# Optimization experiments

Measured on AMD Instinct MI355X. Metric: run time of the kernel, lower is better.

The kernel has to match this reference:

```python
import jax, jax.numpy as jnp
import numpy as np

B, S, D = 4, 2048, 1024
N_EXPERTS, EXPERT_SIZE = 16, 256
WIDTH = N_EXPERTS * EXPERT_SIZE  # 4096


def setup_inputs() -> dict:
    key = jax.random.key(0)
    k_x, k_w1, k_w2, k_g = jax.random.split(key, 4)
    x = jax.random.normal(k_x, (B, S, D), dtype=jnp.float32)
    # Linear params, fan-in scaled init
    w1 = jax.random.normal(k_w1, (D, WIDTH), dtype=jnp.float32) / np.sqrt(D).astype(np.float32)
    b1 = jnp.zeros((WIDTH,), dtype=jnp.float32)
    w2 = jax.random.normal(k_w2, (WIDTH, D), dtype=jnp.float32) / np.sqrt(WIDTH).astype(np.float32)
    b2 = jnp.zeros((D,), dtype=jnp.float32)
    return {"x": x, "w1": w1, "b1": b1, "w2": w2, "b2": b2}


def reference(x, w1, b1, w2, b2):
    # NOTE: the original module computes expert-choice routing tensors
    # (gate einsum -> topk -> one_hot -> identity matmul 'gather'), but the
    # returned value is ONLY the dense FFN applied to x; all routing results
    # are dead code with no effect on the output. Faithful output math:
    h = jax.nn.relu(jnp.einsum('bsd,dw->bsw', x, w1) + b1)  # [B,S,WIDTH]
    return jnp.einsum('bsw,wd->bsd', h, w2) + b2            # [B,S,D]
```

## Files before the change

### kernel.cpp

```cpp
#include <hip/hip_runtime.h>
#include <hip/hip_bf16.h>


typedef __bf16 bf16;
typedef __bf16 bf16x4 __attribute__((ext_vector_type(4)));
typedef __bf16 bf16x8 __attribute__((ext_vector_type(8)));
typedef float  f32x4  __attribute__((ext_vector_type(4)));

#define BM 256
#define BN 128
#define BK 64

__device__ __forceinline__ void gload_lds16(const bf16* g, bf16* l) {
    __builtin_amdgcn_global_load_lds(
        (const __attribute__((address_space(1))) unsigned int*)g,
        (__attribute__((address_space(3))) unsigned int*)l,
        16, 0, 0);
}

__device__ __forceinline__ void transpose_tile(
    const float* __restrict__ in, bf16* __restrict__ out,
    int K, int N, int bx, int by, int t, bf16 (*tile)[72])
{
    const int k0 = by * 64;
    const int n0 = bx * 64;
    const int lr = t >> 4;
    const int lc = (t & 15) << 2;
#pragma unroll
    for (int p = 0; p < 4; ++p) {
        int k = p * 16 + lr;
        float4 v = *(const float4*)(in + (size_t)(k0 + k) * N + n0 + lc);
        tile[lc + 0][k] = (bf16)v.x;
        tile[lc + 1][k] = (bf16)v.y;
        tile[lc + 2][k] = (bf16)v.z;
        tile[lc + 3][k] = (bf16)v.w;
    }
    __syncthreads();
    const int wr = t >> 3;
    const int wc = (t & 7) << 3;
#pragma unroll
    for (int p = 0; p < 2; ++p) {
        int n = p * 32 + wr;
        *(bf16x8*)(out + (size_t)(n0 + n) * K + k0 + wc) =
            *(const bf16x8*)&tile[n][wc];
    }
}

__global__ __launch_bounds__(256) void prep(
    const float* __restrict__ x,  bf16* __restrict__ xb,
    const float* __restrict__ w1, bf16* __restrict__ w1t,
    const float* __restrict__ w2, bf16* __restrict__ w2t)
{
    __shared__ __align__(16) bf16 tile[64][72];
    const int b = blockIdx.x;
    const int t = threadIdx.x;
    if (b < 8192) {
        int i = b * 256 + t;
        float4 v = ((const float4*)x)[i];
        bf16x4 o;
        o.x = (bf16)v.x; o.y = (bf16)v.y; o.z = (bf16)v.z; o.w = (bf16)v.w;
        ((bf16x4*)xb)[i] = o;
    } else if (b < 9216) {
        int b2 = b - 8192;
        transpose_tile(w1, w1t, 1024, 4096, b2 & 63, b2 >> 6, t, tile);
    } else {
        int b2 = b - 9216;
        transpose_tile(w2, w2t, 4096, 1024, b2 & 15, b2 >> 4, t, tile);
    }
}

template <int FUSE_RELU_BF16>
__global__ __launch_bounds__(256, 2) void gemm_bt(
    const bf16* __restrict__ A, const bf16* __restrict__ Bt,
    const float* __restrict__ bias, void* __restrict__ Cout,
    int M, int N, int K, int nx)
{
    __shared__ __align__(16) bf16 As[BM * BK];
    __shared__ __align__(16) bf16 Bs[BN * BK];

    const int lid = blockIdx.x;
    const int xcd = lid & 7;
    const int j   = lid >> 3;
    const int bx  = j % nx;
    const int by  = (j / nx) * 8 + xcd;

    const int tid  = threadIdx.x;
    const int wave = tid >> 6;
    const int lane = tid & 63;

    const int l8  = lane >> 3;
    const int c8  = lane & 7;
    const int swc = (c8 ^ l8) << 3;
    const size_t K_ = (size_t)K;

    const bf16* gA[8]; const bf16* gB[4];
#pragma unroll
    for (int g = 0; g < 8; ++g)
        gA[g] = A + ((size_t)by * BM + wave * 64 + g * 8 + l8) * K_ + swc;
#pragma unroll
    for (int g = 0; g < 4; ++g)
        gB[g] = Bt + ((size_t)bx * BN + wave * 32 + g * 8 + l8) * K_ + swc;
    bf16* lA0 = &As[(wave * 64) * BK] + lane * 8;
    bf16* lB0 = &Bs[(wave * 32) * BK] + lane * 8;

    const int wm   = (wave >> 1) << 7;
    const int wn   = (wave & 1) << 6;
    const int quad = lane >> 4;
    const int r    = lane & 15;
    const int r7   = lane & 7;

    f32x4 acc[8][4] = {};

    for (int k0 = 0; k0 < K; k0 += BK) {
        __syncthreads();
#pragma unroll
        for (int g = 0; g < 8; ++g) {
            gload_lds16(gA[g], lA0 + g * (8 * BK));
            gA[g] += BK;
        }
#pragma unroll
        for (int g = 0; g < 4; ++g) {
            gload_lds16(gB[g], lB0 + g * (8 * BK));
            gB[g] += BK;
        }
        __syncthreads();

#pragma unroll
        for (int h = 0; h < 2; ++h) {
            const int ch = ((h * 4 + quad) ^ r7) << 3;
            bf16x8 bfr[4];
#pragma unroll
            for (int jj = 0; jj < 4; ++jj)
                bfr[jj] = *(const bf16x8*)&Bs[(wn + jj * 16 + r) * BK + ch];
#pragma unroll
            for (int i = 0; i < 8; ++i) {
                bf16x8 af = *(const bf16x8*)&As[(wm + i * 16 + r) * BK + ch];
#pragma unroll
                for (int jj = 0; jj < 4; ++jj)
                    acc[i][jj] = __builtin_amdgcn_mfma_f32_16x16x32_bf16(
                        af, bfr[jj], acc[i][jj], 0, 0, 0);
            }
        }
    }

    const int m_base = by * BM + wm + quad * 4;
    const int n_base = bx * BN + wn + r;
    float bv[4];
#pragma unroll
    for (int jj = 0; jj < 4; ++jj) bv[jj] = bias[n_base + jj * 16];

    if (FUSE_RELU_BF16) {
        bf16* Cb = (bf16*)Cout;
#pragma unroll
        for (int i = 0; i < 8; ++i) {
#pragma unroll
            for (int p = 0; p < 4; ++p) {
                size_t row = (size_t)(m_base + i * 16 + p) * (size_t)N;
#pragma unroll
                for (int jj = 0; jj < 4; ++jj) {
                    float v = acc[i][jj][p] + bv[jj];
                    v = v > 0.f ? v : 0.f;
                    Cb[row + n_base + jj * 16] = (bf16)v;
                }
            }
        }
    } else {
        float* Cf = (float*)Cout;
#pragma unroll
        for (int i = 0; i < 8; ++i) {
#pragma unroll
            for (int p = 0; p < 4; ++p) {
                size_t row = (size_t)(m_base + i * 16 + p) * (size_t)N;
#pragma unroll
                for (int jj = 0; jj < 4; ++jj) {
                    Cf[row + n_base + jj * 16] = acc[i][jj][p] + bv[jj];
                }
            }
        }
    }
}

extern "C" void kernel_launch(void* const* d_in, const int* in_sizes, int n_in,
                              void* d_out, int out_size, void* d_ws, size_t ws_size,
                              hipStream_t stream)
{
    const float* x  = (const float*)d_in[0];
    const float* w1 = (const float*)d_in[1];
    const float* b1 = (const float*)d_in[2];
    const float* w2 = (const float*)d_in[3];
    const float* b2 = (const float*)d_in[4];
    float* out = (float*)d_out;

    const int M = 8192, D = 1024, W = 4096;

    char* ws = (char*)d_ws;
    bf16* xb  = (bf16*)(ws);
    bf16* w1t = (bf16*)(ws + (size_t)(16 << 20));
    bf16* w2t = (bf16*)(ws + (size_t)(24 << 20));
    bf16* h   = (bf16*)(ws + (size_t)(32 << 20));

    prep<<<8192 + 1024 + 1024, 256, 0, stream>>>(x, xb, w1, w1t, w2, w2t);

    gemm_bt<1><<<(W / BN) * (M / BM), 256, 0, stream>>>(
        xb, w1t, b1, (void*)h, M, W, D, W / BN);

    gemm_bt<0><<<(D / BN) * (M / BM), 256, 0, stream>>>(
        h, w2t, b2, (void*)out, M, D, W, D / BN);
}
```

Baseline: 263.6 us.

## Fuse x fp32-to-bf16 conversion into first GEMM and shrink block tile

Drops the separate conversion of x to bf16 from the prep kernel. The first GEMM now loads fp32 x into registers, converts it and writes it to LDS, with the next tile prefetched into registers during compute. The block tile shrinks from 256 to 128 rows, launch bounds rise to 3 blocks per CU, and the XCD-aware block remapping gives way to a plain 2D grid. This saves one pass over x in global memory but turns A into a register-staged load rather than a direct-to-LDS one, lowers reuse per block, and may hurt L2 locality.

```diff
diff --git a/kernel.cpp b/kernel.cpp
--- a/kernel.cpp
+++ b/kernel.cpp
@@ -3,11 +3,10 @@
 
 
 typedef __bf16 bf16;
-typedef __bf16 bf16x4 __attribute__((ext_vector_type(4)));
 typedef __bf16 bf16x8 __attribute__((ext_vector_type(8)));
 typedef float  f32x4  __attribute__((ext_vector_type(4)));
 
-#define BM 256
+#define BM 128
 #define BN 128
 #define BK 64
 
@@ -47,42 +46,31 @@
 }
 
 __global__ __launch_bounds__(256) void prep(
-    const float* __restrict__ x,  bf16* __restrict__ xb,
     const float* __restrict__ w1, bf16* __restrict__ w1t,
     const float* __restrict__ w2, bf16* __restrict__ w2t)
 {
     __shared__ __align__(16) bf16 tile[64][72];
     const int b = blockIdx.x;
     const int t = threadIdx.x;
-    if (b < 8192) {
-        int i = b * 256 + t;
-        float4 v = ((const float4*)x)[i];
-        bf16x4 o;
-        o.x = (bf16)v.x; o.y = (bf16)v.y; o.z = (bf16)v.z; o.w = (bf16)v.w;
-        ((bf16x4*)xb)[i] = o;
-    } else if (b < 9216) {
-        int b2 = b - 8192;
-        transpose_tile(w1, w1t, 1024, 4096, b2 & 63, b2 >> 6, t, tile);
+    if (b < 1024) {
+        transpose_tile(w1, w1t, 1024, 4096, b & 63, b >> 6, t, tile);
     } else {
-        int b2 = b - 9216;
+        int b2 = b - 1024;
         transpose_tile(w2, w2t, 4096, 1024, b2 & 15, b2 >> 4, t, tile);
     }
 }
 
-template <int FUSE_RELU_BF16>
-__global__ __launch_bounds__(256, 2) void gemm_bt(
-    const bf16* __restrict__ A, const bf16* __restrict__ Bt,
+template <int FUSE_RELU_BF16, int A_F32>
+__global__ __launch_bounds__(256, 3) void gemm_bt(
+    const void* __restrict__ Ain, const bf16* __restrict__ Bt,
     const float* __restrict__ bias, void* __restrict__ Cout,
-    int M, int N, int K, int nx)
+    int M, int N, int K)
 {
     __shared__ __align__(16) bf16 As[BM * BK];
     __shared__ __align__(16) bf16 Bs[BN * BK];
 
-    const int lid = blockIdx.x;
-    const int xcd = lid & 7;
-    const int j   = lid >> 3;
-    const int bx  = j % nx;
-    const int by  = (j / nx) * 8 + xcd;
+    const int bx = blockIdx.x;
+    const int by = blockIdx.y;
 
     const int tid  = threadIdx.x;
     const int wave = tid >> 6;
@@ -93,30 +81,70 @@
     const int swc = (c8 ^ l8) << 3;
     const size_t K_ = (size_t)K;
 
-    const bf16* gA[8]; const bf16* gB[4];
-#pragma unroll
-    for (int g = 0; g < 8; ++g)
-        gA[g] = A + ((size_t)by * BM + wave * 64 + g * 8 + l8) * K_ + swc;
+    const bf16* gB[4];
 #pragma unroll
     for (int g = 0; g < 4; ++g)
         gB[g] = Bt + ((size_t)bx * BN + wave * 32 + g * 8 + l8) * K_ + swc;
-    bf16* lA0 = &As[(wave * 64) * BK] + lane * 8;
     bf16* lB0 = &Bs[(wave * 32) * BK] + lane * 8;
 
-    const int wm   = (wave >> 1) << 7;
+    const float* pA32;
+    const bf16*  gA[4];
+    int wofsA = 0;
+    if (A_F32) {
+        pA32 = (const float*)Ain +
+               ((size_t)by * BM + wave * 32 + l8) * K_ + c8 * 8;
+        wofsA = (wave * 32 + l8) * BK + ((c8 ^ l8) << 3);
+    } else {
+#pragma unroll
+        for (int g = 0; g < 4; ++g)
+            gA[g] = (const bf16*)Ain +
+                    ((size_t)by * BM + wave * 32 + g * 8 + l8) * K_ + swc;
+    }
+    bf16* lA0 = &As[(wave * 32) * BK] + lane * 8;
+
+    const int wm   = (wave >> 1) << 6;
     const int wn   = (wave & 1) << 6;
     const int quad = lane >> 4;
     const int r    = lane & 15;
     const int r7   = lane & 7;
 
-    f32x4 acc[8][4] = {};
-
-    for (int k0 = 0; k0 < K; k0 += BK) {
+    f32x4 acc[4][4] = {};
+    float4 rlo[4], rhi[4];
+
+    auto gloadA32 = [&]() {
+#pragma unroll
+        for (int g = 0; g < 4; ++g) {
+            const float* p = pA32 + (size_t)(g * 8) * K_;
+            rlo[g] = *(const float4*)(p);
+            rhi[g] = *(const float4*)(p + 4);
+        }
+        pA32 += BK;
+    };
+    auto writeA32 = [&]() {
+#pragma unroll
+        for (int g = 0; g < 4; ++g) {
+            bf16x8 o;
+            o[0] = (bf16)rlo[g].x; o[1] = (bf16)rlo[g].y;
+            o[2] = (bf16)rlo[g].z; o[3] = (bf16)rlo[g].w;
+            o[4] = (bf16)rhi[g].x; o[5] = (bf16)rhi[g].y;
+            o[6] = (bf16)rhi[g].z; o[7] = (bf16)rhi[g].w;
+            *(bf16x8*)&As[wofsA + g * (8 * BK)] = o;
+        }
+    };
+
+    const int T = K / BK;
+    if (A_F32) gloadA32();
+
+    for (int t = 0; t < T; ++t) {
         __syncthreads();
-#pragma unroll
-        for (int g = 0; g < 8; ++g) {
-            gload_lds16(gA[g], lA0 + g * (8 * BK));
-            gA[g] += BK;
+        if (A_F32) {
+            writeA32();
+        } else {
+#pragma unroll
+            for (int g = 0; g < 4; ++g) {
+                gload_lds16(gA[g], lA0 + g * (8 * BK));
+                gA[g] += BK;
+            }
         }
 #pragma unroll
         for (int g = 0; g < 4; ++g) {
@@ -124,22 +152,24 @@
             gB[g] += BK;
         }
         __syncthreads();
+        if (A_F32 && t + 1 < T) gloadA32();
 
 #pragma unroll
         for (int h = 0; h < 2; ++h) {
             const int ch = ((h * 4 + quad) ^ r7) << 3;
-            bf16x8 bfr[4];
+            bf16x8 af[4], bfr[4];
+#pragma unroll
+            for (int i = 0; i < 4; ++i)
+                af[i] = *(const bf16x8*)&As[(wm + i * 16 + r) * BK + ch];
 #pragma unroll
             for (int jj = 0; jj < 4; ++jj)
                 bfr[jj] = *(const bf16x8*)&Bs[(wn + jj * 16 + r) * BK + ch];
 #pragma unroll
-            for (int i = 0; i < 8; ++i) {
-                bf16x8 af = *(const bf16x8*)&As[(wm + i * 16 + r) * BK + ch];
+            for (int i = 0; i < 4; ++i)
 #pragma unroll
                 for (int jj = 0; jj < 4; ++jj)
                     acc[i][jj] = __builtin_amdgcn_mfma_f32_16x16x32_bf16(
-                        af, bfr[jj], acc[i][jj], 0, 0, 0);
-            }
+                        af[i], bfr[jj], acc[i][jj], 0, 0, 0);
         }
     }
 
@@ -152,7 +182,7 @@
     if (FUSE_RELU_BF16) {
         bf16* Cb = (bf16*)Cout;
 #pragma unroll
-        for (int i = 0; i < 8; ++i) {
+        for (int i = 0; i < 4; ++i) {
 #pragma unroll
             for (int p = 0; p < 4; ++p) {
                 size_t row = (size_t)(m_base + i * 16 + p) * (size_t)N;
@@ -167,7 +197,7 @@
     } else {
         float* Cf = (float*)Cout;
 #pragma unroll
-        for (int i = 0; i < 8; ++i) {
+        for (int i = 0; i < 4; ++i) {
 #pragma unroll
             for (int p = 0; p < 4; ++p) {
                 size_t row = (size_t)(m_base + i * 16 + p) * (size_t)N;
@@ -194,16 +224,15 @@
     const int M = 8192, D = 1024, W = 4096;
 
     char* ws = (char*)d_ws;
-    bf16* xb  = (bf16*)(ws);
-    bf16* w1t = (bf16*)(ws + (size_t)(16 << 20));
-    bf16* w2t = (bf16*)(ws + (size_t)(24 << 20));
-    bf16* h   = (bf16*)(ws + (size_t)(32 << 20));
-
-    prep<<<8192 + 1024 + 1024, 256, 0, stream>>>(x, xb, w1, w1t, w2, w2t);
-
-    gemm_bt<1><<<(W / BN) * (M / BM), 256, 0, stream>>>(
-        xb, w1t, b1, (void*)h, M, W, D, W / BN);
-
-    gemm_bt<0><<<(D / BN) * (M / BM), 256, 0, stream>>>(
-        h, w2t, b2, (void*)out, M, D, W, D / BN);
-}
+    bf16* h   = (bf16*)(ws);
+    bf16* w1t = (bf16*)(ws + (size_t)(64 << 20));
+    bf16* w2t = (bf16*)(ws + (size_t)(72 << 20));
+
+    prep<<<1024 + 1024, 256, 0, stream>>>(w1, w1t, w2, w2t);
+
+    gemm_bt<1, 1><<<dim3(W / BN, M / BM), 256, 0, stream>>>(
+        (const void*)x, w1t, b1, (void*)h, M, W, D);
+
+    gemm_bt<0, 0><<<dim3(D / BN, M / BM), 256, 0, stream>>>(
+        (const void*)h, w2t, b2, (void*)out, M, D, W);
+}
```

After: 287.9 us. 9.2% more time.
